# Performance work log

Hardware: AMD Instinct MI355X
Metric: run time of the kernel (lower is better)

## Reference

```python
import jax, jax.numpy as jnp
import numpy as np
import math

GAIN = 6.0
FREQ = 1000.0
Q = 0.707
SAMPLE_RATE = 44100


def _peaking_coeffs():
    # torchaudio.functional.equalizer_biquad coefficients (peaking EQ)
    w0 = 2.0 * math.pi * FREQ / SAMPLE_RATE
    A = math.exp(GAIN / 40.0 * math.log(10.0))
    alpha = math.sin(w0) / (2.0 * Q)
    b0 = 1.0 + alpha * A
    b1 = -2.0 * math.cos(w0)
    b2 = 1.0 - alpha * A
    a0 = 1.0 + alpha / A
    a1 = -2.0 * math.cos(w0)
    a2 = 1.0 - alpha / A
    # normalize by a0 (lfilter semantics)
    return (np.float32(b0 / a0), np.float32(b1 / a0), np.float32(b2 / a0),
            np.float32(a1 / a0), np.float32(a2 / a0))


def setup_inputs() -> dict:
    key = jax.random.key(0)
    x = jax.random.normal(key, (8, 2, 1200000), dtype=jnp.float32)
    return {"x": x}


def _biquad(x):
    # x: [B, C, T]; direct-form-I biquad with zero initial conditions
    b0, b1, b2, a1, a2 = _peaking_coeffs()
    # FIR part, fully vectorized: f[n] = b0*x[n] + b1*x[n-1] + b2*x[n-2]
    xp = jnp.pad(x, ((0, 0), (0, 0), (2, 0)))
    f = b0 * xp[..., 2:] + b1 * xp[..., 1:-1] + b2 * xp[..., :-2]
    # IIR part via scan over time: y[n] = f[n] - a1*y[n-1] - a2*y[n-2]
    f_t = jnp.moveaxis(f, -1, 0)  # [T, B, C]
    y0 = jnp.zeros(x.shape[:-1], dtype=x.dtype)

    def step(carry, ft):
        y1, y2 = carry
        y = ft - a1 * y1 - a2 * y2
        return (y, y1), y

    _, ys = jax.lax.scan(step, (y0, y0), f_t)
    return jnp.moveaxis(ys, 0, -1)  # [B, C, T]


def reference(x):
    return _biquad(x)
```

## Files before the change

### kernel.cpp

```cpp
#include <hip/hip_runtime.h>
#include <math.h>


typedef float f32x4 __attribute__((ext_vector_type(4)));

#define T_LEN 1200000
#define NCH   16
#define L     32
#define NR    64
#define NWARM 4
#define OUT_ROWS (NR - NWARM)
#define OUT_PER_SEG (OUT_ROWS * L)
#define SEGS_PER_CH (T_LEN / OUT_PER_SEG)
#define NSEG (SEGS_PER_CH * NCH)
#define WPB 4
#define NBLOCKS 1024
#define NWAVES (NBLOCKS * WPB)
#define RSTRIDE 36
#define WAVE_LDS (NR * RSTRIDE)

struct Params {
    float b0, b1, b2, a1, a2;
    float lnr, theta, inv_sinth;
    float C[3][4];
};

struct Seg { const float* xc; float* yc; int g0; };

__device__ __forceinline__ Seg mkseg(int s, const float* __restrict__ x,
                                     float* __restrict__ y)
{
    int ch = s / SEGS_PER_CH;
    int si = s - ch * SEGS_PER_CH;
    Seg g;
    g.xc = x + (size_t)ch * T_LEN;
    g.yc = y + (size_t)ch * T_LEN;
    g.g0 = si * OUT_PER_SEG - NWARM * L;
    return g;
}

__device__ __forceinline__ void load_seg(f32x4 r[8], const Seg& s, int lane)
{
    #pragma unroll
    for (int it = 0; it < 8; ++it) {
        int g = s.g0 + (it << 8) + (lane << 2);
        f32x4 v = {0.f, 0.f, 0.f, 0.f};
        if (g >= 0 && g < T_LEN) v = *(const f32x4*)(s.xc + g);
        r[it] = v;
    }
}

__device__ __forceinline__ void stage_seg(float* __restrict__ xs, const f32x4 r[8],
                                          int lane)
{
    const int row0 = lane >> 3, j = (lane & 7) << 2;
    #pragma unroll
    for (int it = 0; it < 8; ++it) {
        int row = (it << 3) + row0;
        *(f32x4*)&xs[row * RSTRIDE + j] = r[it];
    }
}

__device__ __forceinline__ void process_seg(float* __restrict__ xs,
                                            const Seg& s, int lane,
                                            const Params& P,
                                            const float c1r[4], const float c2r[4])
{
    const int base = lane * RSTRIDE;

    float x1 = 0.f, x2 = 0.f;
    if (lane > 0) {
        x1 = xs[base - RSTRIDE + 31];
        x2 = xs[base - RSTRIDE + 30];
    }
    asm volatile("" ::: "memory");

    float v1 = 0.f, v2 = 0.f;
    #pragma unroll
    for (int b = 0; b < 8; ++b) {
        f32x4 xv = *(const f32x4*)&xs[base + (b << 2)];
        f32x4 yv;
        #pragma unroll
        for (int k = 0; k < 4; ++k) {
            float xk = xv[k];
            float f  = fmaf(P.b0, xk, fmaf(P.b1, x1, P.b2 * x2));
            float t2 = fmaf(-P.a2, v2, f);
            float yk = fmaf(-P.a1, v1, t2);
            v2 = v1; v1 = yk;
            x2 = x1; x1 = xk;
            yv[k] = yk;
        }
        *(f32x4*)&xs[base + (b << 2)] = yv;
    }

    float q11 = __shfl_up(v1, 1), q21 = __shfl_up(v2, 1);
    float q12 = __shfl_up(v1, 2), q22 = __shfl_up(v2, 2);
    float q13 = __shfl_up(v1, 3), q23 = __shfl_up(v2, 3);
    float q14 = __shfl_up(v1, 4), q24 = __shfl_up(v2, 4);
    if (lane < 1) { q11 = 0.f; q21 = 0.f; }
    if (lane < 2) { q12 = 0.f; q22 = 0.f; }
    if (lane < 3) { q13 = 0.f; q23 = 0.f; }
    if (lane < 4) { q14 = 0.f; q24 = 0.f; }
    float e1 = q11, e2 = q21;
    e1 = fmaf(P.C[0][0], q12, fmaf(P.C[0][1], q22, e1));
    e2 = fmaf(P.C[0][2], q12, fmaf(P.C[0][3], q22, e2));
    e1 = fmaf(P.C[1][0], q13, fmaf(P.C[1][1], q23, e1));
    e2 = fmaf(P.C[1][2], q13, fmaf(P.C[1][3], q23, e2));
    e1 = fmaf(P.C[2][0], q14, fmaf(P.C[2][1], q24, e1));
    e2 = fmaf(P.C[2][2], q14, fmaf(P.C[2][3], q24, e2));

    const int j0 = (lane << 2) & 31;
    #pragma unroll
    for (int it = 0; it < 8; ++it) {
        int vo = (it << 6) + lane;
        int row = NWARM + (it << 3) + (lane >> 3);
        row = row > 63 ? 63 : row;
        float al = __shfl(e1, row);
        float be = __shfl(e2, row);
        if (vo < OUT_PER_SEG / 4) {
            f32x4 yv = *(const f32x4*)&xs[row * RSTRIDE + j0];
            f32x4 o;
            #pragma unroll
            for (int k = 0; k < 4; ++k)
                o[k] = fmaf(al, c1r[k], fmaf(be, c2r[k], yv[k]));
            int q = (vo << 2) + NWARM * L;
            __builtin_nontemporal_store(o, (f32x4*)(s.yc + s.g0 + q));
        }
    }
}

#define MEMBAR asm volatile("" ::: "memory")

__global__ __launch_bounds__(256, 4) void eq_kernel(const float* __restrict__ x,
                                                    float* __restrict__ y, Params P)
{
    __shared__ __align__(16) float lds[WPB * WAVE_LDS];
    const int lane = threadIdx.x & 63;
    const int wid  = threadIdx.x >> 6;
    float* xs = lds + wid * WAVE_LDS;
    const int w = blockIdx.x * WPB + wid;

    float c1r[4], c2r[4];
    {
        const int t0 = (lane << 2) & 31;
        float ph[5];
        #pragma unroll
        for (int k = 0; k < 5; ++k) {
            int t = t0 - 1 + k;
            ph[k] = (t < 0) ? 0.f
                            : expf(t * P.lnr) * sinf((t + 1) * P.theta) * P.inv_sinth;
        }
        #pragma unroll
        for (int k = 0; k < 4; ++k) {
            c1r[k] = fmaf(-P.a1, ph[k + 1], -P.a2 * ph[k]);
            c2r[k] = -P.a2 * ph[k + 1];
        }
    }

    const Seg s0 = mkseg(w,          x, y);
    const Seg s1 = mkseg(w + NWAVES, x, y);
    const bool has2 = (w + 2 * NWAVES) < NSEG;
    const Seg s2 = mkseg(has2 ? (w + 2 * NWAVES) : w, x, y);

    f32x4 ra[8], rb[8];
    load_seg(ra, s0, lane);
    load_seg(rb, s1, lane);

    stage_seg(xs, ra, lane); MEMBAR;
    process_seg(xs, s0, lane, P, c1r, c2r);
    if (has2) load_seg(ra, s2, lane);

    stage_seg(xs, rb, lane); MEMBAR;
    process_seg(xs, s1, lane, P, c1r, c2r);

    if (has2) {
        stage_seg(xs, ra, lane); MEMBAR;
        process_seg(xs, s2, lane, P, c1r, c2r);
    }
}

extern "C" void kernel_launch(void* const* d_in, const int* in_sizes, int n_in,
                              void* d_out, int out_size, void* d_ws, size_t ws_size,
                              hipStream_t stream) {
    const float* x = (const float*)d_in[0];
    float* y = (float*)d_out;

    double w0    = 2.0 * M_PI * 1000.0 / 44100.0;
    double A     = exp(6.0 / 40.0 * log(10.0));
    double al    = sin(w0) / (2.0 * 0.707);
    double b0 = 1.0 + al * A;
    double b1 = -2.0 * cos(w0);
    double b2 = 1.0 - al * A;
    double a0 = 1.0 + al / A;
    double a1 = -2.0 * cos(w0);
    double a2 = 1.0 - al / A;
    b0 /= a0; b1 /= a0; b2 /= a0; a1 /= a0; a2 /= a0;

    Params P;
    P.b0 = (float)b0; P.b1 = (float)b1; P.b2 = (float)b2;
    P.a1 = (float)a1; P.a2 = (float)a2;

    double r     = sqrt(a2);
    double theta = acos(-a1 / (2.0 * r));
    P.lnr = (float)log(r);
    P.theta = (float)theta;
    P.inv_sinth = (float)(1.0 / sin(theta));

    double m00 = -a1, m01 = -a2, m10 = 1.0, m11 = 0.0;
    for (int s = 0; s < 5; ++s) {
        double t00 = m00 * m00 + m01 * m10;
        double t01 = m00 * m01 + m01 * m11;
        double t10 = m10 * m00 + m11 * m10;
        double t11 = m10 * m01 + m11 * m11;
        m00 = t00; m01 = t01; m10 = t10; m11 = t11;
    }
    double p00 = m00, p01 = m01, p10 = m10, p11 = m11;
    for (int k = 0; k < 3; ++k) {
        P.C[k][0] = (float)p00; P.C[k][1] = (float)p01;
        P.C[k][2] = (float)p10; P.C[k][3] = (float)p11;
        double t00 = p00 * m00 + p01 * m10;
        double t01 = p00 * m01 + p01 * m11;
        double t10 = p10 * m00 + p11 * m10;
        double t11 = p10 * m01 + p11 * m11;
        p00 = t00; p01 = t01; p10 = t10; p11 = t11;
    }

    eq_kernel<<<NBLOCKS, 256, 0, stream>>>(x, y, P);
}
```

Before: 29.82 us.

## Use one segment per wave with direct per-lane loads, skipping LDS staging

Replaces the persistent three-segments-per-wave software pipeline with a grid of one segment per wave (NSEG/WPB blocks). Each lane now loads its own 32 contiguous samples straight into registers instead of loading coalesced and staging through LDS, and takes the previous-row history by shuffle. Output stores become ordinary stores instead of nontemporal ones. This removes the LDS staging pass and the per-wave prologue cost, but per-lane strided 128B loads are less coalesced and the explicit overlap of loads with compute across segments is lost.

```diff
diff --git a/kernel.cpp b/kernel.cpp
--- a/kernel.cpp
+++ b/kernel.cpp
@@ -14,8 +14,7 @@
 #define SEGS_PER_CH (T_LEN / OUT_PER_SEG)
 #define NSEG (SEGS_PER_CH * NCH)
 #define WPB 4
-#define NBLOCKS 1024
-#define NWAVES (NBLOCKS * WPB)
+#define NBLOCKS (NSEG / WPB)
 #define RSTRIDE 36
 #define WAVE_LDS (NR * RSTRIDE)
 
@@ -25,60 +24,58 @@
     float C[3][4];
 };
 
-struct Seg { const float* xc; float* yc; int g0; };
+__global__ __launch_bounds__(256, 4) void eq_kernel(const float* __restrict__ x,
+                                                    float* __restrict__ y, Params P)
+{
+    __shared__ __align__(16) float lds[WPB * WAVE_LDS];
+    const int lane = threadIdx.x & 63;
+    const int wid  = threadIdx.x >> 6;
+    float* ys = lds + wid * WAVE_LDS;
 
-__device__ __forceinline__ Seg mkseg(int s, const float* __restrict__ x,
-                                     float* __restrict__ y)
-{
-    int ch = s / SEGS_PER_CH;
-    int si = s - ch * SEGS_PER_CH;
-    Seg g;
-    g.xc = x + (size_t)ch * T_LEN;
-    g.yc = y + (size_t)ch * T_LEN;
-    g.g0 = si * OUT_PER_SEG - NWARM * L;
-    return g;
-}
+    const int s  = blockIdx.x * WPB + wid;
+    const int ch = s / SEGS_PER_CH;
+    const int si = s - ch * SEGS_PER_CH;
+    const float* __restrict__ xc = x + (size_t)ch * T_LEN;
+    float*       __restrict__ yc = y + (size_t)ch * T_LEN;
+    const int g0 = si * OUT_PER_SEG - NWARM * L;
 
-__device__ __forceinline__ void load_seg(f32x4 r[8], const Seg& s, int lane)
-{
-    #pragma unroll
-    for (int it = 0; it < 8; ++it) {
-        int g = s.g0 + (it << 8) + (lane << 2);
-        f32x4 v = {0.f, 0.f, 0.f, 0.f};
-        if (g >= 0 && g < T_LEN) v = *(const f32x4*)(s.xc + g);
-        r[it] = v;
+    float c1r[4], c2r[4];
+    {
+        const int t0 = (lane << 2) & 31;
+        float ph[5];
+        #pragma unroll
+        for (int k = 0; k < 5; ++k) {
+            int t = t0 - 1 + k;
+            ph[k] = (t < 0) ? 0.f
+                            : expf(t * P.lnr) * sinf((t + 1) * P.theta) * P.inv_sinth;
+        }
+        #pragma unroll
+        for (int k = 0; k < 4; ++k) {
+            c1r[k] = fmaf(-P.a1, ph[k + 1], -P.a2 * ph[k]);
+            c2r[k] = -P.a2 * ph[k + 1];
+        }
     }
-}
 
-__device__ __forceinline__ void stage_seg(float* __restrict__ xs, const f32x4 r[8],
-                                          int lane)
-{
-    const int row0 = lane >> 3, j = (lane & 7) << 2;
-    #pragma unroll
-    for (int it = 0; it < 8; ++it) {
-        int row = (it << 3) + row0;
-        *(f32x4*)&xs[row * RSTRIDE + j] = r[it];
+    f32x4 r[8];
+    {
+        const int gl = g0 + (lane << 5);
+        #pragma unroll
+        for (int k = 0; k < 8; ++k) {
+            int g = gl + (k << 2);
+            f32x4 v = {0.f, 0.f, 0.f, 0.f};
+            if (g >= 0 && g < T_LEN) v = *(const f32x4*)(xc + g);
+            r[k] = v;
+        }
     }
-}
 
-__device__ __forceinline__ void process_seg(float* __restrict__ xs,
-                                            const Seg& s, int lane,
-                                            const Params& P,
-                                            const float c1r[4], const float c2r[4])
-{
+    float x1 = __shfl_up(r[7].w, 1);
+    float x2 = __shfl_up(r[7].z, 1);
+    if (lane == 0) { x1 = 0.f; x2 = 0.f; }
+    float v1 = 0.f, v2 = 0.f;
     const int base = lane * RSTRIDE;
-
-    float x1 = 0.f, x2 = 0.f;
-    if (lane > 0) {
-        x1 = xs[base - RSTRIDE + 31];
-        x2 = xs[base - RSTRIDE + 30];
-    }
-    asm volatile("" ::: "memory");
-
-    float v1 = 0.f, v2 = 0.f;
     #pragma unroll
     for (int b = 0; b < 8; ++b) {
-        f32x4 xv = *(const f32x4*)&xs[base + (b << 2)];
+        f32x4 xv = r[b];
         f32x4 yv;
         #pragma unroll
         for (int k = 0; k < 4; ++k) {
@@ -90,7 +87,7 @@
             x2 = x1; x1 = xk;
             yv[k] = yk;
         }
-        *(f32x4*)&xs[base + (b << 2)] = yv;
+        *(f32x4*)&ys[base + (b << 2)] = yv;
     }
 
     float q11 = __shfl_up(v1, 1), q21 = __shfl_up(v2, 1);
@@ -118,64 +115,14 @@
         float al = __shfl(e1, row);
         float be = __shfl(e2, row);
         if (vo < OUT_PER_SEG / 4) {
-            f32x4 yv = *(const f32x4*)&xs[row * RSTRIDE + j0];
+            f32x4 yv = *(const f32x4*)&ys[row * RSTRIDE + j0];
             f32x4 o;
             #pragma unroll
             for (int k = 0; k < 4; ++k)
                 o[k] = fmaf(al, c1r[k], fmaf(be, c2r[k], yv[k]));
             int q = (vo << 2) + NWARM * L;
-            __builtin_nontemporal_store(o, (f32x4*)(s.yc + s.g0 + q));
+            *(f32x4*)(yc + g0 + q) = o;
         }
-    }
-}
-
-#define MEMBAR asm volatile("" ::: "memory")
-
-__global__ __launch_bounds__(256, 4) void eq_kernel(const float* __restrict__ x,
-                                                    float* __restrict__ y, Params P)
-{
-    __shared__ __align__(16) float lds[WPB * WAVE_LDS];
-    const int lane = threadIdx.x & 63;
-    const int wid  = threadIdx.x >> 6;
-    float* xs = lds + wid * WAVE_LDS;
-    const int w = blockIdx.x * WPB + wid;
-
-    float c1r[4], c2r[4];
-    {
-        const int t0 = (lane << 2) & 31;
-        float ph[5];
-        #pragma unroll
-        for (int k = 0; k < 5; ++k) {
-            int t = t0 - 1 + k;
-            ph[k] = (t < 0) ? 0.f
-                            : expf(t * P.lnr) * sinf((t + 1) * P.theta) * P.inv_sinth;
-        }
-        #pragma unroll
-        for (int k = 0; k < 4; ++k) {
-            c1r[k] = fmaf(-P.a1, ph[k + 1], -P.a2 * ph[k]);
-            c2r[k] = -P.a2 * ph[k + 1];
-        }
-    }
-
-    const Seg s0 = mkseg(w,          x, y);
-    const Seg s1 = mkseg(w + NWAVES, x, y);
-    const bool has2 = (w + 2 * NWAVES) < NSEG;
-    const Seg s2 = mkseg(has2 ? (w + 2 * NWAVES) : w, x, y);
-
-    f32x4 ra[8], rb[8];
-    load_seg(ra, s0, lane);
-    load_seg(rb, s1, lane);
-
-    stage_seg(xs, ra, lane); MEMBAR;
-    process_seg(xs, s0, lane, P, c1r, c2r);
-    if (has2) load_seg(ra, s2, lane);
-
-    stage_seg(xs, rb, lane); MEMBAR;
-    process_seg(xs, s1, lane, P, c1r, c2r);
-
-    if (has2) {
-        stage_seg(xs, ra, lane); MEMBAR;
-        process_seg(xs, s2, lane, P, c1r, c2r);
     }
 }
 
```

Result: slower. 30.74 us (+3.1%).
